# Performance work log

Measured on AMD Instinct MI355X. Metric: run time of the kernel, lower is better.

Reference implementation:

```python
import jax, jax.numpy as jnp
import numpy as np

NUM_EXPERTS = 8
D_MODEL = 1024
VOCAB = 32000
BATCH = 4096


def setup_inputs() -> dict:
    key = jax.random.key(0)
    kx, kp, kw, kb = jax.random.split(key, 4)
    x = jax.random.normal(kx, (BATCH, D_MODEL), dtype=jnp.float32)
    pointer_addresses = jax.random.randint(kp, (BATCH,), 0, 1000000, dtype=jnp.int64)
    # Per-expert Linear params, xavier-ish scale: weight [E, V, d], bias [E, V]
    scale = float(np.sqrt(6.0 / (D_MODEL + VOCAB)))
    W = jax.random.uniform(kw, (NUM_EXPERTS, VOCAB, D_MODEL), dtype=jnp.float32,
                           minval=-scale, maxval=scale)
    b = jnp.zeros((NUM_EXPERTS, VOCAB), dtype=jnp.float32)
    return {"x": x, "pointer_addresses": pointer_addresses, "W": W, "b": b}


def reference(x, pointer_addresses, W, b):
    # expert_index = pointer % num_experts  (all rows route to exactly one expert)
    num_experts = W.shape[0]
    expidx = pointer_addresses.astype(jnp.int32) % num_experts  # [B]
    out = jnp.zeros((x.shape[0], W.shape[1]), dtype=W.dtype)    # [B, V]
    # Fixed small loop over experts (structurally distinct weights).
    # Masked dense GEMM + combine, matching masked gather/Linear/scatter math.
    for e in range(num_experts):
        ye = jnp.einsum('bd,vd->bv', x, W[e]) + b[e]            # [B, V]
        out = out + jnp.where((expidx == e)[:, None], ye, jnp.zeros((), dtype=W.dtype))
    return out
```

## Files before the change

### kernel.cpp

```cpp
#include <hip/hip_runtime.h>
#include <hip/hip_bf16.h>

#define NEXP  8
#define DM    1024
#define VOCAB 32000
#define BATCH 4096
#define TM    128
#define TN    128
#define BK    32

typedef short bf16x8 __attribute__((ext_vector_type(8)));
typedef float f32x4  __attribute__((ext_vector_type(4)));

__global__ void route_kernel(const int* __restrict__ ptr,
                             int* __restrict__ gstart,
                             int* __restrict__ perm)
{
    __shared__ int cnt[NEXP];
    __shared__ int cur[NEXP];
    int tid = threadIdx.x;
    if (tid < NEXP) cnt[tid] = 0;
    __syncthreads();
    for (int r = tid; r < BATCH; r += blockDim.x) {
        int e = ptr[r] & (NEXP - 1);
        atomicAdd(&cnt[e], 1);
    }
    __syncthreads();
    if (tid == 0) {
        int acc = 0;
        for (int e = 0; e < NEXP; ++e) {
            gstart[e] = acc;
            cur[e] = acc;
            acc += cnt[e];
        }
        gstart[NEXP] = acc;
    }
    __syncthreads();
    for (int r = tid; r < BATCH; r += blockDim.x) {
        int e = ptr[r] & (NEXP - 1);
        int pos = atomicAdd(&cur[e], 1);
        perm[pos] = r;
    }
}

__global__ void pack_kernel(const float* __restrict__ x,
                            const int* __restrict__ perm,
                            __hip_bfloat16* __restrict__ Ap)
{
    int p   = blockIdx.x;
    int tid = threadIdx.x;
    __hip_bfloat16* dst = Ap + (size_t)p * DM + tid * 4;
    if (p >= BATCH) {
        *(unsigned long long*)dst = 0ull;
        return;
    }
    int r = perm[p];
    const float4 v = *(const float4*)(x + (size_t)r * DM + tid * 4);
    union { __hip_bfloat162 h[2]; unsigned long long q; } cv;
    cv.h[0] = __float22bfloat162_rn(make_float2(v.x, v.y));
    cv.h[1] = __float22bfloat162_rn(make_float2(v.z, v.w));
    *(unsigned long long*)dst = cv.q;
}

__global__ __launch_bounds__(256) void moe_gemm_kernel(
    const __hip_bfloat16* __restrict__ Ap,
    const float* __restrict__ W,
    const float* __restrict__ bias,
    const int* __restrict__ gstart,
    const int* __restrict__ perm,
    float* __restrict__ out)
{
    const int nt = blockIdx.x;
    const int e  = blockIdx.y;
    const int g0 = gstart[e];
    const int ne = gstart[e + 1] - g0;
    if (ne <= 0) return;
    const int nmt = (ne + TM - 1) / TM;
    const int n0  = nt * TN;

    __shared__ __hip_bfloat16 Asm[TM * BK];
    __shared__ __hip_bfloat16 Bsm[TN * BK];

    const int tid  = threadIdx.x;
    const int lane = tid & 63;
    const int wave = tid >> 6;
    const int wm   = (wave & 1) * 64;
    const int wn   = (wave >> 1) * 64;
    const int l16  = lane & 15;
    const int quad = lane >> 4;

    const int arow = wave * 16 + (lane >> 2);
    const int acol = (lane & 3) * 8;

    const float* Wb = W + ((size_t)e * VOCAB + n0) * DM;

    float bj[4];
    #pragma unroll
    for (int j = 0; j < 4; ++j)
        bj[j] = bias[(size_t)e * VOCAB + n0 + wn + j * 16 + l16];

    for (int mt = 0; mt < nmt; ++mt) {
        const int m0 = mt * TM;
        const __hip_bfloat16* Ab = Ap + (size_t)(g0 + m0) * DM;
        f32x4 acc[4][4] = {};

        for (int k0 = 0; k0 < DM; k0 += BK) {
            __syncthreads();
            #pragma unroll
            for (int t = 0; t < 2; ++t) {
                const __hip_bfloat16* src = Ab + (size_t)(t * 64 + arow) * DM + k0 + acol;
                __builtin_amdgcn_global_load_lds(
                    (const __attribute__((address_space(1))) void*)src,
                    (__attribute__((address_space(3))) void*)(Asm + (t * 64 + wave * 16) * BK),
                    16, 0, 0);
            }
            #pragma unroll
            for (int t = 0; t < 4; ++t) {
                int u   = t * 256 + tid;
                int row = u >> 3;
                int c4  = (u & 7) * 4;
                const float4 v = *(const float4*)(Wb + (size_t)row * DM + k0 + c4);
                union { __hip_bfloat162 h[2]; unsigned long long q; } cv;
                cv.h[0] = __float22bfloat162_rn(make_float2(v.x, v.y));
                cv.h[1] = __float22bfloat162_rn(make_float2(v.z, v.w));
                *(unsigned long long*)(Bsm + row * BK + c4) = cv.q;
            }
            __syncthreads();
            bf16x8 av[4], bv[4];
            #pragma unroll
            for (int i = 0; i < 4; ++i)
                av[i] = *(const bf16x8*)(Asm + (wm + i * 16 + l16) * BK + quad * 8);
            #pragma unroll
            for (int j = 0; j < 4; ++j)
                bv[j] = *(const bf16x8*)(Bsm + (wn + j * 16 + l16) * BK + quad * 8);
            #pragma unroll
            for (int i = 0; i < 4; ++i) {
                #pragma unroll
                for (int j = 0; j < 4; ++j) {
                    acc[i][j] = __builtin_amdgcn_mfma_f32_16x16x32_bf16(
                        av[i], bv[j], acc[i][j], 0, 0, 0);
                }
            }
        }

        #pragma unroll
        for (int j = 0; j < 4; ++j) {
            const int col = n0 + wn + j * 16 + l16;
            const float bv_ = bj[j];
            #pragma unroll
            for (int i = 0; i < 4; ++i) {
                #pragma unroll
                for (int r = 0; r < 4; ++r) {
                    int pr = m0 + wm + i * 16 + quad * 4 + r;
                    if (pr < ne) {
                        int orow = perm[g0 + pr];
                        out[(size_t)orow * VOCAB + col] = acc[i][j][r] + bv_;
                    }
                }
            }
        }
    }
}

extern "C" void kernel_launch(void* const* d_in, const int* in_sizes, int n_in,
                              void* d_out, int out_size, void* d_ws, size_t ws_size,
                              hipStream_t stream)
{
    const float* x   = (const float*)d_in[0];
    const int*   ptr = (const int*)d_in[1];
    const float* W   = (const float*)d_in[2];
    const float* b   = (const float*)d_in[3];
    float* out = (float*)d_out;

    char* ws = (char*)d_ws;
    int* gstart = (int*)ws;
    int* perm   = (int*)(ws + 64);
    __hip_bfloat16* Ap = (__hip_bfloat16*)(ws + 32768);

    route_kernel<<<1, 256, 0, stream>>>(ptr, gstart, perm);
    pack_kernel<<<BATCH + TM, 256, 0, stream>>>(x, perm, Ap);
    dim3 grid(VOCAB / TN, NEXP);
    moe_gemm_kernel<<<grid, 256, 0, stream>>>(Ap, W, b, gstart, perm, out);
}
```

Baseline: 2.480 ms.

## Double-buffer LDS tiles and prefetch next K-slice into registers during MFMA

Splits the A and B shared-memory tiles into two buffers. The next K-slice of A is issued via global_load_lds and the next slice of W is loaded into registers while MFMAs run on the current buffer, and only then converted to bf16 and written to LDS. This halves the barriers per K-step and is meant to hide global-load latency behind compute. In exchange it doubles the LDS footprint and holds more live registers for the prefetched W values, which may lower occupancy.

```diff
diff --git a/kernel.cpp b/kernel.cpp
--- a/kernel.cpp
+++ b/kernel.cpp
@@ -8,6 +8,7 @@
 #define TM    128
 #define TN    128
 #define BK    32
+#define NKT   (DM / BK)
 
 typedef short bf16x8 __attribute__((ext_vector_type(8)));
 typedef float f32x4  __attribute__((ext_vector_type(4)));
@@ -62,6 +63,48 @@
     *(unsigned long long*)dst = cv.q;
 }
 
+#define STAGE_A(DST, KOFF)                                                    \
+    _Pragma("unroll")                                                         \
+    for (int t = 0; t < 2; ++t) {                                             \
+        const __hip_bfloat16* src =                                           \
+            Ab + (size_t)(t * 64 + arow) * DM + (KOFF) + acol;                \
+        __builtin_amdgcn_global_load_lds(                                     \
+            (const __attribute__((address_space(1))) void*)src,               \
+            (__attribute__((address_space(3))) void*)(DST + (t * 64 + wave * 16) * BK), \
+            16, 0, 0);                                                        \
+    }
+
+#define LOAD_B_REG(PV, KOFF)                                                  \
+    _Pragma("unroll")                                                         \
+    for (int t = 0; t < 4; ++t)                                               \
+        PV[t] = *(const float4*)(Wb + (size_t)b_row[t] * DM + (KOFF) + b_c4[t]);
+
+#define WRITE_B_LDS(DST, PV)                                                  \
+    _Pragma("unroll")                                                         \
+    for (int t = 0; t < 4; ++t) {                                             \
+        union { __hip_bfloat162 h2[2]; unsigned long long q; } cv;            \
+        cv.h2[0] = __float22bfloat162_rn(make_float2(PV[t].x, PV[t].y));      \
+        cv.h2[1] = __float22bfloat162_rn(make_float2(PV[t].z, PV[t].w));      \
+        *(unsigned long long*)(DST + b_row[t] * BK + b_c4[t]) = cv.q;         \
+    }
+
+#define COMPUTE(SRCA, SRCB)                                                   \
+    {                                                                         \
+        bf16x8 av[4], bv[4];                                                  \
+        _Pragma("unroll")                                                     \
+        for (int i = 0; i < 4; ++i)                                           \
+            av[i] = *(const bf16x8*)(SRCA + (wm + i * 16 + l16) * BK + quad * 8); \
+        _Pragma("unroll")                                                     \
+        for (int j = 0; j < 4; ++j)                                           \
+            bv[j] = *(const bf16x8*)(SRCB + (wn + j * 16 + l16) * BK + quad * 8); \
+        _Pragma("unroll")                                                     \
+        for (int i = 0; i < 4; ++i)                                           \
+            _Pragma("unroll")                                                 \
+            for (int j = 0; j < 4; ++j)                                       \
+                acc[i][j] = __builtin_amdgcn_mfma_f32_16x16x32_bf16(          \
+                    av[i], bv[j], acc[i][j], 0, 0, 0);                        \
+    }
+
 __global__ __launch_bounds__(256) void moe_gemm_kernel(
     const __hip_bfloat16* __restrict__ Ap,
     const float* __restrict__ W,
@@ -78,8 +121,10 @@
     const int nmt = (ne + TM - 1) / TM;
     const int n0  = nt * TN;
 
-    __shared__ __hip_bfloat16 Asm[TM * BK];
-    __shared__ __hip_bfloat16 Bsm[TN * BK];
+    __shared__ __hip_bfloat16 Asm0[TM * BK];
+    __shared__ __hip_bfloat16 Asm1[TM * BK];
+    __shared__ __hip_bfloat16 Bsm0[TN * BK];
+    __shared__ __hip_bfloat16 Bsm1[TN * BK];
 
     const int tid  = threadIdx.x;
     const int lane = tid & 63;
@@ -92,6 +137,14 @@
     const int arow = wave * 16 + (lane >> 2);
     const int acol = (lane & 3) * 8;
 
+    int b_row[4], b_c4[4];
+    #pragma unroll
+    for (int t = 0; t < 4; ++t) {
+        int u = t * 256 + tid;
+        b_row[t] = u >> 3;
+        b_c4[t]  = (u & 7) * 4;
+    }
+
     const float* Wb = W + ((size_t)e * VOCAB + n0) * DM;
 
     float bj[4];
@@ -103,44 +156,29 @@
         const int m0 = mt * TM;
         const __hip_bfloat16* Ab = Ap + (size_t)(g0 + m0) * DM;
         f32x4 acc[4][4] = {};
-
-        for (int k0 = 0; k0 < DM; k0 += BK) {
+        float4 pv[4];
+
+        STAGE_A(Asm0, 0)
+        LOAD_B_REG(pv, 0)
+        WRITE_B_LDS(Bsm0, pv)
+        __syncthreads();
+
+        for (int kh = 0; kh < NKT / 2; ++kh) {
+            const int ke = 2 * kh + 1;
+            STAGE_A(Asm1, ke * BK)
+            LOAD_B_REG(pv, ke * BK)
+            COMPUTE(Asm0, Bsm0)
+            WRITE_B_LDS(Bsm1, pv)
             __syncthreads();
-            #pragma unroll
-            for (int t = 0; t < 2; ++t) {
-                const __hip_bfloat16* src = Ab + (size_t)(t * 64 + arow) * DM + k0 + acol;
-                __builtin_amdgcn_global_load_lds(
-                    (const __attribute__((address_space(1))) void*)src,
-                    (__attribute__((address_space(3))) void*)(Asm + (t * 64 + wave * 16) * BK),
-                    16, 0, 0);
+            if (kh + 1 < NKT / 2) {
+                STAGE_A(Asm0, (ke + 1) * BK)
+                LOAD_B_REG(pv, (ke + 1) * BK)
             }
-            #pragma unroll
-            for (int t = 0; t < 4; ++t) {
-                int u   = t * 256 + tid;
-                int row = u >> 3;
-                int c4  = (u & 7) * 4;
-                const float4 v = *(const float4*)(Wb + (size_t)row * DM + k0 + c4);
-                union { __hip_bfloat162 h[2]; unsigned long long q; } cv;
-                cv.h[0] = __float22bfloat162_rn(make_float2(v.x, v.y));
-                cv.h[1] = __float22bfloat162_rn(make_float2(v.z, v.w));
-                *(unsigned long long*)(Bsm + row * BK + c4) = cv.q;
+            COMPUTE(Asm1, Bsm1)
+            if (kh + 1 < NKT / 2) {
+                WRITE_B_LDS(Bsm0, pv)
             }
             __syncthreads();
-            bf16x8 av[4], bv[4];
-            #pragma unroll
-            for (int i = 0; i < 4; ++i)
-                av[i] = *(const bf16x8*)(Asm + (wm + i * 16 + l16) * BK + quad * 8);
-            #pragma unroll
-            for (int j = 0; j < 4; ++j)
-                bv[j] = *(const bf16x8*)(Bsm + (wn + j * 16 + l16) * BK + quad * 8);
-            #pragma unroll
-            for (int i = 0; i < 4; ++i) {
-                #pragma unroll
-                for (int j = 0; j < 4; ++j) {
-                    acc[i][j] = __builtin_amdgcn_mfma_f32_16x16x32_bf16(
-                        av[i], bv[j], acc[i][j], 0, 0, 0);
-                }
-            }
         }
 
         #pragma unroll
```

Result: slower. 2.605 ms (+5.0%).
